# Performance work log

Hardware: AMD Instinct MI355X
Metric: run time of the kernel (lower is better)

The kernel has to match this reference:

```python
import jax, jax.numpy as jnp
import numpy as np

H = 8          # num heads
HD = 64        # head dim
DV = 512       # values_dim
DC = 128       # coords_dim
DI = 512       # att_inner_dim
DF = 2048      # mlp inner dim


def _ln(x, g, b, eps=1e-5):
    mu = jnp.mean(x, -1, keepdims=True)
    var = jnp.mean((x - mu) ** 2, -1, keepdims=True)
    return (x - mu) * jax.lax.rsqrt(var + eps) * g + b


def _rms(x, g, eps=1e-6):
    return x * jax.lax.rsqrt(jnp.mean(x * x, -1, keepdims=True) + eps) * g


def _heads(x):  # b n (h d) -> b h n d
    b, n, _ = x.shape
    return x.reshape(b, n, H, HD).transpose(0, 2, 1, 3)


def setup_inputs() -> dict:
    key = jax.random.key(0)
    ks = iter(jax.random.split(key, 40))
    r = lambda shape, s=0.02: jax.random.normal(next(ks), shape, jnp.float32) * s
    inp = {
        'coords': jax.random.normal(next(ks), (4, 4096, DC), jnp.float32),
        'values': jax.random.normal(next(ks), (4, 4096, DV), jnp.float32),
        'Lv': jax.random.normal(next(ks), (4, 1024, DV), jnp.float32),
        'Lc': jax.random.normal(next(ks), (4, 1024, DC), jnp.float32),
        'lam': jax.random.normal(next(ks), (1,), jnp.float32),
        'lvn_g': jnp.ones((DV,)), 'lvn_b': jnp.zeros((DV,)),
        'lcn_g': jnp.ones((DC,)), 'lcn_b': jnp.zeros((DC,)),
        'ck_w': r((DC, DI)), 'ck_b': jnp.zeros((DI,)), 'ck_g': jnp.ones((DI,)),
        'cq_w': r((DC, DI)), 'cq_b': jnp.zeros((DI,)), 'cq_g': jnp.ones((DI,)),
        'vq_w': r((DV, DI)), 'vq_b': jnp.zeros((DI,)), 'vq_g': jnp.ones((DI,)),
        'vk_w': r((DV, 2 * DI)), 'vk_b': jnp.zeros((2 * DI,)),
        'op_w': r((DI, DV)), 'op_b': jnp.zeros((DV,)),
        'oln_g': jnp.ones((DV,)), 'oln_b': jnp.zeros((DV,)),
        'm1_w': r((DV, DF)), 'm1_b': jnp.zeros((DF,)),
        'm2_w': r((DF, DF)), 'm2_b': jnp.zeros((DF,)),
        'm3_w': r((DF, DV)), 'm3_b': jnp.zeros((DV,)),
    }
    return inp


def reference(coords, values, Lv, Lc, lam, lvn_g, lvn_b, lcn_g, lcn_b,
              ck_w, ck_b, ck_g, cq_w, cq_b, cq_g, vq_w, vq_b, vq_g,
              vk_w, vk_b, op_w, op_b, oln_g, oln_b,
              m1_w, m1_b, m2_w, m2_b, m3_w, m3_b):
    Lv = _ln(Lv, lvn_g, lvn_b)
    Lc = _ln(Lc, lcn_g, lcn_b)
    vk = Lv @ vk_w + vk_b                     # [b, nl, 2*DI]
    v_v, k_v = jnp.split(vk, 2, axis=-1)
    k_c = _rms(Lc @ ck_w + ck_b, ck_g)
    k_c, v_v, k_v = _heads(k_c), _heads(v_v), _heads(k_v)  # [b,h,nl,d]
    q_v = _heads(_rms(values @ vq_w + vq_b, vq_g))         # [b,h,nq,d]
    q_c = _heads(_rms(coords @ cq_w + cq_b, cq_g))
    # dual-score attention
    scores = jnp.einsum('bhnd,bhmd->bhnm', q_c, k_c) \
        + lam[0] * jnp.einsum('bhnd,bhmd->bhnm', q_v, k_v)
    scores = scores / np.float32(np.sqrt(HD))
    attn = jax.nn.softmax(scores, axis=-1)
    V_out = jnp.einsum('bhnm,bhmd->bhnd', attn, v_v)       # [b,h,nq,d]
    b, _, nq, _ = V_out.shape
    V_out = V_out.transpose(0, 2, 1, 3).reshape(b, nq, DI)
    V_out = V_out @ op_w + op_b
    # (LayerNorm, MLP) head: Linear-GELU-Linear-GELU-Linear
    h = _ln(V_out, oln_g, oln_b)
    h = jax.nn.gelu(h @ m1_w + m1_b)
    h = jax.nn.gelu(h @ m2_w + m2_b)
    return h @ m3_w + m3_b
```

## Files before the change

### kernel.cpp

```cpp
#include <hip/hip_runtime.h>
#include <cstdint>
#include <cstddef>

typedef __bf16 bf16_t;
typedef __bf16 bf16x8 __attribute__((ext_vector_type(8)));
typedef __bf16 bf16x4 __attribute__((ext_vector_type(4)));
typedef float  f32x4  __attribute__((ext_vector_type(4)));
typedef float  f32x16 __attribute__((ext_vector_type(16)));

typedef __attribute__((address_space(1))) void gvoid_t;
typedef __attribute__((address_space(3))) void lvoid_t;

__device__ __forceinline__ f32x4 mfma16(bf16x8 a, bf16x8 b, f32x4 c) {
  return __builtin_amdgcn_mfma_f32_16x16x32_bf16(a, b, c, 0, 0, 0);
}
__device__ __forceinline__ f32x16 mfma32(bf16x8 a, bf16x8 b, f32x16 c) {
  return __builtin_amdgcn_mfma_f32_32x32x16_bf16(a, b, c, 0, 0, 0);
}

__device__ __forceinline__ void async_copy16(const void* g, void* l) {
  __builtin_amdgcn_global_load_lds((gvoid_t*)g, (lvoid_t*)l, 16, 0, 0);
}

__device__ __forceinline__ float gelu_tanh(float x) {
  float u = 0.7978845608028654f * (x + 0.044715f * x * x * x);
  float e = exp2f(2.8853900817779268f * u);
  float t = 1.f - 2.f / (e + 1.f);
  return 0.5f * x * (1.f + t);
}

struct TransBatch {
  const float* src[8];
  bf16_t* dst[8];
  int K[8], N[8], bx[8], base[8];
};

__global__ void transpose_batch_kernel(TransBatch d) {
  int id = blockIdx.x;
  int mi = 0;
#pragma unroll
  for (int j = 1; j < 8; j++)
    if (id >= d.base[j]) mi = j;
  int local = id - d.base[mi];
  int bxw = d.bx[mi];
  int n0 = (local % bxw) * 32, k0 = (local / bxw) * 32;
  const float* in = d.src[mi];
  bf16_t* out = d.dst[mi];
  int K = d.K[mi], N = d.N[mi];

  __shared__ float t[32][33];
  int tx = threadIdx.x, ty = threadIdx.y;
#pragma unroll
  for (int i = 0; i < 4; i++)
    t[ty + i * 8][tx] = in[(size_t)(k0 + ty + i * 8) * N + n0 + tx];
  __syncthreads();
#pragma unroll
  for (int i = 0; i < 4; i++)
    out[(size_t)(n0 + ty + i * 8) * K + k0 + tx] = (bf16_t)t[tx][ty + i * 8];
}

__global__ void transpose_v_kernel(const bf16_t* __restrict__ vk, bf16_t* __restrict__ vt) {
  __shared__ bf16_t t[32][33];
  int b = blockIdx.z;
  int d0 = blockIdx.x * 32, m0 = blockIdx.y * 32;
  int tx = threadIdx.x, ty = threadIdx.y;
#pragma unroll
  for (int i = 0; i < 4; i++)
    t[ty + i * 8][tx] = vk[((size_t)b * 1024 + m0 + ty + i * 8) * 1024 + d0 + tx];
  __syncthreads();
#pragma unroll
  for (int i = 0; i < 4; i++)
    vt[((size_t)b * 512 + d0 + ty + i * 8) * 1024 + m0 + tx] = t[tx][ty + i * 8];
}

__global__ void cvt2_bf16_kernel(const float* __restrict__ a, bf16_t* __restrict__ oa, int n4a,
                                 const float* __restrict__ b, bf16_t* __restrict__ ob, int n4b) {
  int i = blockIdx.x * blockDim.x + threadIdx.x;
  const float* s;
  bf16_t* o;
  int j;
  if (i < n4a) { s = a; o = oa; j = i; }
  else { j = i - n4a; if (j >= n4b) return; s = b; o = ob; }
  float4 v = ((const float4*)s)[j];
  bf16x4 r = {(bf16_t)v.x, (bf16_t)v.y, (bf16_t)v.z, (bf16_t)v.w};
  ((bf16x4*)o)[j] = r;
}

template <int D>
__global__ void ln_kernel(const float* __restrict__ x, const float* __restrict__ g,
                          const float* __restrict__ bb, bf16_t* __restrict__ out) {
  int row = blockIdx.x, t = threadIdx.x;
  float v = x[(size_t)row * D + t];
  float s = v, s2 = v * v;
#pragma unroll
  for (int o = 32; o > 0; o >>= 1) { s += __shfl_xor(s, o); s2 += __shfl_xor(s2, o); }
  __shared__ float rs[8], rs2[8];
  constexpr int NW = D / 64;
  int w = t >> 6;
  if ((t & 63) == 0) { rs[w] = s; rs2[w] = s2; }
  __syncthreads();
  if (t < 64) {
    float a = (t < NW) ? rs[t] : 0.f;
    float a2 = (t < NW) ? rs2[t] : 0.f;
#pragma unroll
    for (int o = 4; o > 0; o >>= 1) { a += __shfl_xor(a, o); a2 += __shfl_xor(a2, o); }
    if (t == 0) { rs[0] = a; rs2[0] = a2; }
  }
  __syncthreads();
  float mu = rs[0] * (1.f / D);
  float var = rs2[0] * (1.f / D) - mu * mu;
  float rr = rsqrtf(var + 1e-5f);
  out[(size_t)row * D + t] = (bf16_t)((v - mu) * rr * g[t] + bb[t]);
}

__global__ void rms_kernel(const float* __restrict__ x, const float* __restrict__ g,
                           bf16_t* __restrict__ out) {
  int row = blockIdx.x, t = threadIdx.x;
  float v = x[(size_t)row * 512 + t];
  float s2 = v * v;
#pragma unroll
  for (int o = 32; o > 0; o >>= 1) s2 += __shfl_xor(s2, o);
  __shared__ float rs2[8];
  int w = t >> 6;
  if ((t & 63) == 0) rs2[w] = s2;
  __syncthreads();
  if (t < 64) {
    float a = (t < 8) ? rs2[t] : 0.f;
#pragma unroll
    for (int o = 4; o > 0; o >>= 1) a += __shfl_xor(a, o);
    if (t == 0) rs2[0] = a;
  }
  __syncthreads();
  float r = rsqrtf(rs2[0] * (1.f / 512.f) + 1e-6f);
  out[(size_t)row * 512 + t] = (bf16_t)(v * r * g[t]);
}

template <int EPI>
__global__ __launch_bounds__(256, 2) void gemm_bt(
    const bf16_t* __restrict__ A, const bf16_t* __restrict__ Bt,
    const float* __restrict__ bias, void* __restrict__ outp,
    int M, int N, int K) {
  __shared__ __align__(16) bf16_t As[128 * 32];
  __shared__ __align__(16) bf16_t Bs[128 * 32];
  const int tid = threadIdx.x;
  const int lane = tid & 63, wv = tid >> 6;
  const int half = lane >> 5, l32 = lane & 31;
  const int m_base = blockIdx.y * 128, n_base = blockIdx.x * 128;
  const int wm = wv & 1, wn = wv >> 1;
  f32x16 acc[2][2] = {};

  for (int k0 = 0; k0 < K; k0 += 32) {
#pragma unroll
    for (int c = 0; c < 2; c++) {
      int p = c * 256 + tid;
      int row = p >> 2;
      int kc = (p & 3) ^ ((row >> 1) & 3);
      async_copy16(&A[(size_t)(m_base + row) * K + k0 + kc * 8], &As[(size_t)p * 8]);
      async_copy16(&Bt[(size_t)(n_base + row) * K + k0 + kc * 8], &Bs[(size_t)p * 8]);
    }
    __syncthreads();
    bf16x8 af[2][2], bfr[2][2];
#pragma unroll
    for (int mi = 0; mi < 2; mi++)
#pragma unroll
      for (int ks = 0; ks < 2; ks++) {
        int r = wm * 64 + mi * 32 + l32;
        int g = ks * 2 + half;
        af[mi][ks] = *(const bf16x8*)&As[(size_t)(r * 4 + (g ^ ((r >> 1) & 3))) * 8];
      }
#pragma unroll
    for (int ni = 0; ni < 2; ni++)
#pragma unroll
      for (int ks = 0; ks < 2; ks++) {
        int r = wn * 64 + ni * 32 + l32;
        int g = ks * 2 + half;
        bfr[ni][ks] = *(const bf16x8*)&Bs[(size_t)(r * 4 + (g ^ ((r >> 1) & 3))) * 8];
      }
#pragma unroll
    for (int ks = 0; ks < 2; ks++)
#pragma unroll
      for (int mi = 0; mi < 2; mi++)
#pragma unroll
        for (int ni = 0; ni < 2; ni++)
          acc[mi][ni] = mfma32(af[mi][ks], bfr[ni][ks], acc[mi][ni]);
    __syncthreads();
  }

#pragma unroll
  for (int mi = 0; mi < 2; mi++)
#pragma unroll
    for (int ni = 0; ni < 2; ni++) {
      int n = n_base + wn * 64 + ni * 32 + l32;
      float bv = bias[n];
#pragma unroll
      for (int r = 0; r < 16; r++) {
        int row = (r & 3) + 8 * (r >> 2) + 4 * half;
        int m = m_base + wm * 64 + mi * 32 + row;
        float v = acc[mi][ni][r] + bv;
        if (EPI == 2) v = gelu_tanh(v);
        if (EPI == 0) ((float*)outp)[(size_t)m * N + n] = v;
        else          ((bf16_t*)outp)[(size_t)m * N + n] = (bf16_t)v;
      }
    }
}

__global__ __launch_bounds__(256, 2) void attn_kernel(
    const bf16_t* __restrict__ qc, const bf16_t* __restrict__ qv,
    const bf16_t* __restrict__ kcb, const bf16_t* __restrict__ vkb,
    const bf16_t* __restrict__ vt, const float* __restrict__ lamp,
    bf16_t* __restrict__ vout) {
  const int b = blockIdx.z, h = blockIdx.y;
  const int tid = threadIdx.x;
  const int lane = tid & 63, wv = tid >> 6;
  const int quad = lane >> 4, l16 = lane & 15;
  const int qrow0 = blockIdx.x * 128 + wv * 32;
  const float SCL = 0.125f * 1.4426950408889634f;
  const float C1 = SCL, C2 = lamp[0] * SCL;

  __shared__ __align__(16) bf16_t kcS[64 * 64];
  __shared__ __align__(16) bf16_t kvS[64 * 64];
  __shared__ __align__(16) bf16_t vtS[64 * 64];
  __shared__ __align__(16) bf16_t sP[4][32 * 64];
  bf16_t* sPw = sP[wv];

  bf16x8 qcf[2][2], qvf[2][2];
#pragma unroll
  for (int mt = 0; mt < 2; mt++)
#pragma unroll
    for (int ks = 0; ks < 2; ks++) {
      size_t o = ((size_t)b * 4096 + qrow0 + mt * 16 + l16) * 512 + h * 64 + ks * 32 + quad * 8;
      qcf[mt][ks] = *(const bf16x8*)&qc[o];
      qvf[mt][ks] = *(const bf16x8*)&qv[o];
    }

  f32x4 O[2][4] = {};
  float ls[2][4] = {};

  for (int kb = 0; kb < 16; kb++) {
#pragma unroll
    for (int i = 0; i < 2; i++) {
      int p = i * 256 + tid;
      int row = p >> 3;
      int gc = (p & 7) ^ (row & 7);
      async_copy16(&kcb[((size_t)b * 1024 + kb * 64 + row) * 512 + h * 64 + gc * 8],
                   &kcS[(size_t)p * 8]);
      async_copy16(&vkb[((size_t)b * 1024 + kb * 64 + row) * 1024 + 512 + h * 64 + gc * 8],
                   &kvS[(size_t)p * 8]);
      async_copy16(&vt[((size_t)((b * 8 + h) * 64) + row) * 1024 + kb * 64 + gc * 8],
                   &vtS[(size_t)p * 8]);
    }
    __syncthreads();

#pragma unroll
    for (int nt = 0; nt < 4; nt++) {
      int krow = nt * 16 + l16;
      int kb8 = krow & 7;
      bf16x8 kc0 = *(const bf16x8*)&kcS[(size_t)(krow * 8 + (quad ^ kb8)) * 8];
      bf16x8 kc1 = *(const bf16x8*)&kcS[(size_t)(krow * 8 + ((4 + quad) ^ kb8)) * 8];
      bf16x8 kv0 = *(const bf16x8*)&kvS[(size_t)(krow * 8 + (quad ^ kb8)) * 8];
      bf16x8 kv1 = *(const bf16x8*)&kvS[(size_t)(krow * 8 + ((4 + quad) ^ kb8)) * 8];
#pragma unroll
      for (int mt = 0; mt < 2; mt++) {
        f32x4 sc = {};
        sc = mfma16(qcf[mt][0], kc0, sc);
        sc = mfma16(qcf[mt][1], kc1, sc);
        f32x4 sv = {};
        sv = mfma16(qvf[mt][0], kv0, sv);
        sv = mfma16(qvf[mt][1], kv1, sv);
#pragma unroll
        for (int r = 0; r < 4; r++) {
          float p = exp2f(sc[r] * C1 + sv[r] * C2);
          ls[mt][r] += p;
          int prow = mt * 16 + quad * 4 + r;
          int col = nt * 16 + l16;
          sPw[prow * 64 + (((col >> 3) ^ (prow & 7)) * 8) + (col & 7)] = (bf16_t)p;
        }
      }
    }
    asm volatile("s_waitcnt lgkmcnt(0)" ::: "memory");

#pragma unroll
    for (int ks2 = 0; ks2 < 2; ks2++) {
      bf16x8 pa[2];
#pragma unroll
      for (int mt = 0; mt < 2; mt++) {
        int prow = mt * 16 + l16;
        pa[mt] = *(const bf16x8*)&sPw[(size_t)(prow * 8 + ((ks2 * 4 + quad) ^ (prow & 7))) * 8];
      }
#pragma unroll
      for (int ntd = 0; ntd < 4; ntd++) {
        int drow = ntd * 16 + l16;
        bf16x8 vb = *(const bf16x8*)&vtS[(size_t)(drow * 8 + ((ks2 * 4 + quad) ^ (drow & 7))) * 8];
        O[0][ntd] = mfma16(pa[0], vb, O[0][ntd]);
        O[1][ntd] = mfma16(pa[1], vb, O[1][ntd]);
      }
    }
    __syncthreads();
  }

#pragma unroll
  for (int mt = 0; mt < 2; mt++) {
    float inv[4];
#pragma unroll
    for (int r = 0; r < 4; r++) {
      float v = ls[mt][r];
      v += __shfl_xor(v, 1);
      v += __shfl_xor(v, 2);
      v += __shfl_xor(v, 4);
      v += __shfl_xor(v, 8);
      inv[r] = 1.f / v;
    }
#pragma unroll
    for (int ntd = 0; ntd < 4; ntd++)
#pragma unroll
      for (int r = 0; r < 4; r++) {
        size_t o = ((size_t)b * 4096 + qrow0 + mt * 16 + quad * 4 + r) * 512 + h * 64 + ntd * 16 + l16;
        vout[o] = (bf16_t)(O[mt][ntd][r] * inv[r]);
      }
  }
}

extern "C" void kernel_launch(void* const* d_in, const int* in_sizes, int n_in,
                              void* d_out, int out_size, void* d_ws, size_t ws_size,
                              hipStream_t stream) {
  (void)in_sizes; (void)n_in; (void)out_size; (void)ws_size;
  const float* coords = (const float*)d_in[0];
  const float* values = (const float*)d_in[1];
  const float* Lv     = (const float*)d_in[2];
  const float* Lc     = (const float*)d_in[3];
  const float* lam    = (const float*)d_in[4];
  const float* lvn_g  = (const float*)d_in[5];
  const float* lvn_b  = (const float*)d_in[6];
  const float* lcn_g  = (const float*)d_in[7];
  const float* lcn_b  = (const float*)d_in[8];
  const float* ck_w = (const float*)d_in[9];  const float* ck_b = (const float*)d_in[10]; const float* ck_g = (const float*)d_in[11];
  const float* cq_w = (const float*)d_in[12]; const float* cq_b = (const float*)d_in[13]; const float* cq_g = (const float*)d_in[14];
  const float* vq_w = (const float*)d_in[15]; const float* vq_b = (const float*)d_in[16]; const float* vq_g = (const float*)d_in[17];
  const float* vk_w = (const float*)d_in[18]; const float* vk_b = (const float*)d_in[19];
  const float* op_w = (const float*)d_in[20]; const float* op_b = (const float*)d_in[21];
  const float* oln_g = (const float*)d_in[22]; const float* oln_b = (const float*)d_in[23];
  const float* m1_w = (const float*)d_in[24]; const float* m1_b = (const float*)d_in[25];
  const float* m2_w = (const float*)d_in[26]; const float* m2_b = (const float*)d_in[27];
  const float* m3_w = (const float*)d_in[28]; const float* m3_b = (const float*)d_in[29];

  char* ws = (char*)d_ws;
  size_t off = 0;
  auto alloc = [&](size_t bytes) { void* p = ws + off; off += (bytes + 255) & ~(size_t)255; return p; };

  bf16_t* wt_m1 = (bf16_t*)alloc((size_t)512 * 2048 * 2);
  bf16_t* wt_m2 = (bf16_t*)alloc((size_t)2048 * 2048 * 2);
  bf16_t* wt_m3 = (bf16_t*)alloc((size_t)2048 * 512 * 2);
  float*  scr0  = (float*) alloc((size_t)16384 * 512 * 4);
  bf16_t* qv_bf = (bf16_t*)alloc((size_t)16384 * 512 * 2);
  bf16_t* qc_bf = (bf16_t*)alloc((size_t)16384 * 512 * 2);
  bf16_t* voutb = (bf16_t*)alloc((size_t)16384 * 512 * 2);
  bf16_t* h0    = (bf16_t*)alloc((size_t)16384 * 512 * 2);
  bf16_t* h1    = (bf16_t*)alloc((size_t)16384 * 2048 * 2);
  bf16_t* h2    = (bf16_t*)alloc((size_t)16384 * 2048 * 2);

  size_t ov = (size_t)((char*)h1 - ws);
  auto oalloc = [&](size_t bytes) { void* p = ws + ov; ov += (bytes + 255) & ~(size_t)255; return p; };
  bf16_t* wt_vk = (bf16_t*)oalloc((size_t)1024 * 512 * 2);
  bf16_t* wt_ck = (bf16_t*)oalloc((size_t)512 * 128 * 2);
  bf16_t* wt_cq = (bf16_t*)oalloc((size_t)512 * 128 * 2);
  bf16_t* wt_vq = (bf16_t*)oalloc((size_t)512 * 512 * 2);
  bf16_t* wt_op = (bf16_t*)oalloc((size_t)512 * 512 * 2);
  bf16_t* lv_ln = (bf16_t*)oalloc((size_t)4096 * 512 * 2);
  bf16_t* lc_ln = (bf16_t*)oalloc((size_t)4096 * 128 * 2);
  bf16_t* vkob  = (bf16_t*)oalloc((size_t)4096 * 1024 * 2);
  float*  kc_f  = (float*) oalloc((size_t)4096 * 512 * 4);
  bf16_t* kc_bf = (bf16_t*)oalloc((size_t)4096 * 512 * 2);
  bf16_t* val_bf= (bf16_t*)oalloc((size_t)16384 * 512 * 2);
  bf16_t* crd_bf= (bf16_t*)oalloc((size_t)16384 * 128 * 2);
  bf16_t* vt    = (bf16_t*)oalloc((size_t)4 * 512 * 1024 * 2);

  TransBatch tb8;
  const float* srcs[8] = {vk_w, ck_w, cq_w, vq_w, op_w, m1_w, m2_w, m3_w};
  bf16_t* dsts[8] = {wt_vk, wt_ck, wt_cq, wt_vq, wt_op, wt_m1, wt_m2, wt_m3};
  int Ks[8] = {512, 128, 128, 512, 512, 512, 2048, 2048};
  int Ns[8] = {1024, 512, 512, 512, 512, 2048, 2048, 512};
  int cum = 0;
  for (int i = 0; i < 8; i++) {
    tb8.src[i] = srcs[i]; tb8.dst[i] = dsts[i];
    tb8.K[i] = Ks[i]; tb8.N[i] = Ns[i];
    tb8.bx[i] = Ns[i] / 32;
    tb8.base[i] = cum;
    cum += (Ns[i] / 32) * (Ks[i] / 32);
  }
  transpose_batch_kernel<<<cum, dim3(32, 8), 0, stream>>>(tb8);

  cvt2_bf16_kernel<<<(16384 * 512 / 4 + 16384 * 128 / 4 + 255) / 256, 256, 0, stream>>>(
      values, val_bf, 16384 * 512 / 4, coords, crd_bf, 16384 * 128 / 4);

  ln_kernel<512><<<4096, 512, 0, stream>>>(Lv, lvn_g, lvn_b, lv_ln);
  ln_kernel<128><<<4096, 128, 0, stream>>>(Lc, lcn_g, lcn_b, lc_ln);

  gemm_bt<1><<<dim3(8, 32), 256, 0, stream>>>(lv_ln, wt_vk, vk_b, vkob, 4096, 1024, 512);
  gemm_bt<0><<<dim3(4, 32), 256, 0, stream>>>(lc_ln, wt_ck, ck_b, kc_f, 4096, 512, 128);
  rms_kernel<<<4096, 512, 0, stream>>>(kc_f, ck_g, kc_bf);

  gemm_bt<0><<<dim3(4, 128), 256, 0, stream>>>(val_bf, wt_vq, vq_b, scr0, 16384, 512, 512);
  rms_kernel<<<16384, 512, 0, stream>>>(scr0, vq_g, qv_bf);
  gemm_bt<0><<<dim3(4, 128), 256, 0, stream>>>(crd_bf, wt_cq, cq_b, scr0, 16384, 512, 128);
  rms_kernel<<<16384, 512, 0, stream>>>(scr0, cq_g, qc_bf);

  transpose_v_kernel<<<dim3(16, 32, 4), dim3(32, 8), 0, stream>>>(vkob, vt);

  attn_kernel<<<dim3(32, 8, 4), 256, 0, stream>>>(qc_bf, qv_bf, kc_bf, vkob, vt, lam, voutb);

  gemm_bt<0><<<dim3(4, 128), 256, 0, stream>>>(voutb, wt_op, op_b, scr0, 16384, 512, 512);
  ln_kernel<512><<<16384, 512, 0, stream>>>(scr0, oln_g, oln_b, h0);

  gemm_bt<2><<<dim3(16, 128), 256, 0, stream>>>(h0, wt_m1, m1_b, h1, 16384, 2048, 512);
  gemm_bt<2><<<dim3(16, 128), 256, 0, stream>>>(h1, wt_m2, m2_b, h2, 16384, 2048, 2048);
  gemm_bt<0><<<dim3(4, 128), 256, 0, stream>>>(h2, wt_m3, m3_b, (float*)d_out, 16384, 512, 2048);
}
```

Measured before the change: 726.5 us.

## Switch GEMMs to 16x16 MFMA and add 64-row tile kernel for narrow GEMMs

```diff
diff --git a/kernel.cpp b/kernel.cpp
--- a/kernel.cpp
+++ b/kernel.cpp
@@ -6,16 +6,12 @@
 typedef __bf16 bf16x8 __attribute__((ext_vector_type(8)));
 typedef __bf16 bf16x4 __attribute__((ext_vector_type(4)));
 typedef float  f32x4  __attribute__((ext_vector_type(4)));
-typedef float  f32x16 __attribute__((ext_vector_type(16)));
 
 typedef __attribute__((address_space(1))) void gvoid_t;
 typedef __attribute__((address_space(3))) void lvoid_t;
 
 __device__ __forceinline__ f32x4 mfma16(bf16x8 a, bf16x8 b, f32x4 c) {
   return __builtin_amdgcn_mfma_f32_16x16x32_bf16(a, b, c, 0, 0, 0);
-}
-__device__ __forceinline__ f32x16 mfma32(bf16x8 a, bf16x8 b, f32x16 c) {
-  return __builtin_amdgcn_mfma_f32_32x32x16_bf16(a, b, c, 0, 0, 0);
 }
 
 __device__ __forceinline__ void async_copy16(const void* g, void* l) {
@@ -144,10 +140,10 @@
   __shared__ __align__(16) bf16_t Bs[128 * 32];
   const int tid = threadIdx.x;
   const int lane = tid & 63, wv = tid >> 6;
-  const int half = lane >> 5, l32 = lane & 31;
+  const int quad = lane >> 4, l16 = lane & 15;
   const int m_base = blockIdx.y * 128, n_base = blockIdx.x * 128;
   const int wm = wv & 1, wn = wv >> 1;
-  f32x16 acc[2][2] = {};
+  f32x4 acc[4][4] = {};
 
   for (int k0 = 0; k0 < K; k0 += 32) {
 #pragma unroll
@@ -159,49 +155,111 @@
       async_copy16(&Bt[(size_t)(n_base + row) * K + k0 + kc * 8], &Bs[(size_t)p * 8]);
     }
     __syncthreads();
-    bf16x8 af[2][2], bfr[2][2];
+    bf16x8 af[4], bfr[4];
+#pragma unroll
+    for (int mi = 0; mi < 4; mi++) {
+      int r = wm * 64 + mi * 16 + l16;
+      int kc = quad ^ ((r >> 1) & 3);
+      af[mi] = *(const bf16x8*)&As[(size_t)(r * 4 + kc) * 8];
+    }
+#pragma unroll
+    for (int ni = 0; ni < 4; ni++) {
+      int r = wn * 64 + ni * 16 + l16;
+      int kc = quad ^ ((r >> 1) & 3);
+      bfr[ni] = *(const bf16x8*)&Bs[(size_t)(r * 4 + kc) * 8];
+    }
+#pragma unroll
+    for (int mi = 0; mi < 4; mi++)
+#pragma unroll
+      for (int ni = 0; ni < 4; ni++)
+        acc[mi][ni] = mfma16(af[mi], bfr[ni], acc[mi][ni]);
+    __syncthreads();
+  }
+
+#pragma unroll
+  for (int mi = 0; mi < 4; mi++) {
+    int m = m_base + wm * 64 + mi * 16 + quad * 4;
+#pragma unroll
+    for (int ni = 0; ni < 4; ni++) {
+      int n = n_base + wn * 64 + ni * 16 + l16;
+      float bv = bias[n];
+#pragma unroll
+      for (int r2 = 0; r2 < 4; r2++) {
+        float v = acc[mi][ni][r2] + bv;
+        if (EPI == 2) v = gelu_tanh(v);
+        if (EPI == 0) ((float*)outp)[(size_t)(m + r2) * N + n] = v;
+        else          ((bf16_t*)outp)[(size_t)(m + r2) * N + n] = (bf16_t)v;
+      }
+    }
+  }
+}
+
+template <int EPI>
+__global__ __launch_bounds__(256, 2) void gemm64(
+    const bf16_t* __restrict__ A, const bf16_t* __restrict__ Bt,
+    const float* __restrict__ bias, void* __restrict__ outp,
+    int M, int N, int K) {
+  __shared__ __align__(16) bf16_t As[64 * 32];
+  __shared__ __align__(16) bf16_t Bs[128 * 32];
+  const int tid = threadIdx.x;
+  const int lane = tid & 63, wv = tid >> 6;
+  const int quad = lane >> 4, l16 = lane & 15;
+  const int m_base = blockIdx.y * 64, n_base = blockIdx.x * 128;
+  const int wm = wv & 1, wn = wv >> 1;
+  f32x4 acc[2][4] = {};
+
+  for (int k0 = 0; k0 < K; k0 += 32) {
+    {
+      int p = tid;
+      int row = p >> 2;
+      int kc = (p & 3) ^ ((row >> 1) & 3);
+      async_copy16(&A[(size_t)(m_base + row) * K + k0 + kc * 8], &As[(size_t)p * 8]);
+    }
+#pragma unroll
+    for (int c = 0; c < 2; c++) {
+      int p = c * 256 + tid;
+      int row = p >> 2;
+      int kc = (p & 3) ^ ((row >> 1) & 3);
+      async_copy16(&Bt[(size_t)(n_base + row) * K + k0 + kc * 8], &Bs[(size_t)p * 8]);
+    }
+    __syncthreads();
+    bf16x8 af[2], bfr[4];
+#pragma unroll
+    for (int mi = 0; mi < 2; mi++) {
+      int r = wm * 32 + mi * 16 + l16;
+      int kc = quad ^ ((r >> 1) & 3);
+      af[mi] = *(const bf16x8*)&As[(size_t)(r * 4 + kc) * 8];
+    }
+#pragma unroll
+    for (int ni = 0; ni < 4; ni++) {
+      int r = wn * 64 + ni * 16 + l16;
+      int kc = quad ^ ((r >> 1) & 3);
+      bfr[ni] = *(const bf16x8*)&Bs[(size_t)(r * 4 + kc) * 8];
+    }
 #pragma unroll
     for (int mi = 0; mi < 2; mi++)
 #pragma unroll
-      for (int ks = 0; ks < 2; ks++) {
-        int r = wm * 64 + mi * 32 + l32;
-        int g = ks * 2 + half;
-        af[mi][ks] = *(const bf16x8*)&As[(size_t)(r * 4 + (g ^ ((r >> 1) & 3))) * 8];
-      }
-#pragma unroll
-    for (int ni = 0; ni < 2; ni++)
-#pragma unroll
-      for (int ks = 0; ks < 2; ks++) {
-        int r = wn * 64 + ni * 32 + l32;
-        int g = ks * 2 + half;
-        bfr[ni][ks] = *(const bf16x8*)&Bs[(size_t)(r * 4 + (g ^ ((r >> 1) & 3))) * 8];
-      }
-#pragma unroll
-    for (int ks = 0; ks < 2; ks++)
-#pragma unroll
-      for (int mi = 0; mi < 2; mi++)
-#pragma unroll
-        for (int ni = 0; ni < 2; ni++)
-          acc[mi][ni] = mfma32(af[mi][ks], bfr[ni][ks], acc[mi][ni]);
-    __syncthreads();
-  }
-
-#pragma unroll
-  for (int mi = 0; mi < 2; mi++)
-#pragma unroll
-    for (int ni = 0; ni < 2; ni++) {
-      int n = n_base + wn * 64 + ni * 32 + l32;
+      for (int ni = 0; ni < 4; ni++)
+        acc[mi][ni] = mfma16(af[mi], bfr[ni], acc[mi][ni]);
+    __syncthreads();
+  }
+
+#pragma unroll
+  for (int mi = 0; mi < 2; mi++) {
+    int m = m_base + wm * 32 + mi * 16 + quad * 4;
+#pragma unroll
+    for (int ni = 0; ni < 4; ni++) {
+      int n = n_base + wn * 64 + ni * 16 + l16;
       float bv = bias[n];
 #pragma unroll
-      for (int r = 0; r < 16; r++) {
-        int row = (r & 3) + 8 * (r >> 2) + 4 * half;
-        int m = m_base + wm * 64 + mi * 32 + row;
-        float v = acc[mi][ni][r] + bv;
+      for (int r2 = 0; r2 < 4; r2++) {
+        float v = acc[mi][ni][r2] + bv;
         if (EPI == 2) v = gelu_tanh(v);
-        if (EPI == 0) ((float*)outp)[(size_t)m * N + n] = v;
-        else          ((bf16_t*)outp)[(size_t)m * N + n] = (bf16_t)v;
-      }
-    }
+        if (EPI == 0) ((float*)outp)[(size_t)(m + r2) * N + n] = v;
+        else          ((bf16_t*)outp)[(size_t)(m + r2) * N + n] = (bf16_t)v;
+      }
+    }
+  }
 }
 
 __global__ __launch_bounds__(256, 2) void attn_kernel(
@@ -395,23 +453,23 @@
   ln_kernel<512><<<4096, 512, 0, stream>>>(Lv, lvn_g, lvn_b, lv_ln);
   ln_kernel<128><<<4096, 128, 0, stream>>>(Lc, lcn_g, lcn_b, lc_ln);
 
-  gemm_bt<1><<<dim3(8, 32), 256, 0, stream>>>(lv_ln, wt_vk, vk_b, vkob, 4096, 1024, 512);
-  gemm_bt<0><<<dim3(4, 32), 256, 0, stream>>>(lc_ln, wt_ck, ck_b, kc_f, 4096, 512, 128);
+  gemm64<1><<<dim3(8, 64), 256, 0, stream>>>(lv_ln, wt_vk, vk_b, vkob, 4096, 1024, 512);
+  gemm64<0><<<dim3(4, 64), 256, 0, stream>>>(lc_ln, wt_ck, ck_b, kc_f, 4096, 512, 128);
   rms_kernel<<<4096, 512, 0, stream>>>(kc_f, ck_g, kc_bf);
 
-  gemm_bt<0><<<dim3(4, 128), 256, 0, stream>>>(val_bf, wt_vq, vq_b, scr0, 16384, 512, 512);
+  gemm64<0><<<dim3(4, 256), 256, 0, stream>>>(val_bf, wt_vq, vq_b, scr0, 16384, 512, 512);
   rms_kernel<<<16384, 512, 0, stream>>>(scr0, vq_g, qv_bf);
-  gemm_bt<0><<<dim3(4, 128), 256, 0, stream>>>(crd_bf, wt_cq, cq_b, scr0, 16384, 512, 128);
+  gemm64<0><<<dim3(4, 256), 256, 0, stream>>>(crd_bf, wt_cq, cq_b, scr0, 16384, 512, 128);
   rms_kernel<<<16384, 512, 0, stream>>>(scr0, cq_g, qc_bf);
 
   transpose_v_kernel<<<dim3(16, 32, 4), dim3(32, 8), 0, stream>>>(vkob, vt);
 
   attn_kernel<<<dim3(32, 8, 4), 256, 0, stream>>>(qc_bf, qv_bf, kc_bf, vkob, vt, lam, voutb);
 
-  gemm_bt<0><<<dim3(4, 128), 256, 0, stream>>>(voutb, wt_op, op_b, scr0, 16384, 512, 512);
+  gemm64<0><<<dim3(4, 256), 256, 0, stream>>>(voutb, wt_op, op_b, scr0, 16384, 512, 512);
   ln_kernel<512><<<16384, 512, 0, stream>>>(scr0, oln_g, oln_b, h0);
 
   gemm_bt<2><<<dim3(16, 128), 256, 0, stream>>>(h0, wt_m1, m1_b, h1, 16384, 2048, 512);
   gemm_bt<2><<<dim3(16, 128), 256, 0, stream>>>(h1, wt_m2, m2_b, h2, 16384, 2048, 2048);
-  gemm_bt<0><<<dim3(4, 128), 256, 0, stream>>>(h2, wt_m3, m3_b, (float*)d_out, 16384, 512, 2048);
-}
+  gemm64<0><<<dim3(4, 256), 256, 0, stream>>>(h2, wt_m3, m3_b, (float*)d_out, 16384, 512, 2048);
+}
```

After: 700.7 us. 1.04x faster.
